# Optimization experiments

Hardware: AMD Instinct MI355X
Metric: run time of the kernel (lower is better)

## Reference

```python
import jax, jax.numpy as jnp
import numpy as np

N, E, D_IN, HID, OUT, H = 20000, 320000, 128, 128, 128, 4

def _lin(key, fan_in, fan_out):
    kw, kb = jax.random.split(key)
    W = jax.random.normal(kw, (fan_in, fan_out), jnp.float32) * 0.05
    b = jax.random.normal(kb, (fan_out,), jnp.float32) * 0.05
    return W, b

def setup_inputs() -> dict:
    key = jax.random.key(0)
    ks = jax.random.split(key, 10)
    x = jax.random.normal(ks[0], (N, D_IN), jnp.float32)
    edge_index = jax.random.randint(ks[1], (2, E), 0, N, jnp.int32)
    # Layer 0: TransformerConv(D_IN -> HID, heads=H, concat=True)
    Wq0, bq0 = _lin(ks[2], D_IN, H * HID)
    Wk0, bk0 = _lin(ks[3], D_IN, H * HID)
    Wv0, bv0 = _lin(ks[4], D_IN, H * HID)
    Ws0, bs0 = _lin(ks[5], D_IN, H * HID)   # root/skip projection
    # Layer 1: TransformerConv(H*HID -> OUT, heads=H, concat=False)
    Wq1, bq1 = _lin(ks[6], H * HID, H * OUT)
    Wk1, bk1 = _lin(ks[7], H * HID, H * OUT)
    Wv1, bv1 = _lin(ks[8], H * HID, H * OUT)
    Ws1, bs1 = _lin(ks[9], H * HID, OUT)    # skip maps to OUT when concat=False
    return dict(x=x, edge_index=edge_index,
                Wq0=Wq0, bq0=bq0, Wk0=Wk0, bk0=bk0, Wv0=Wv0, bv0=bv0, Ws0=Ws0, bs0=bs0,
                Wq1=Wq1, bq1=bq1, Wk1=Wk1, bk1=bk1, Wv1=Wv1, bv1=bv1, Ws1=Ws1, bs1=bs1)

def _transformer_conv(x, src, dst, Wq, bq, Wk, bk, Wv, bv, Ws, bs, heads, out_ch, concat):
    n = x.shape[0]
    q = (x @ Wq + bq).reshape(n, heads, out_ch)
    k = (x @ Wk + bk).reshape(n, heads, out_ch)
    v = (x @ Wv + bv).reshape(n, heads, out_ch)
    # per-edge attention logits: [E, H]
    alpha = jnp.einsum('ehc,ehc->eh', q[dst], k[src]) / jnp.sqrt(jnp.float32(out_ch))
    # softmax grouped by destination node (numerically stable)
    m = jax.ops.segment_max(alpha, dst, num_segments=n)        # [N, H]
    alpha = jnp.exp(alpha - m[dst])
    s = jax.ops.segment_sum(alpha, dst, num_segments=n)       # [N, H]
    alpha = alpha / (s[dst] + 1e-16)
    # weighted scatter-add of messages: [N, H, C]
    out = jax.ops.segment_sum(alpha[..., None] * v[src], dst, num_segments=n)
    if concat:
        out = out.reshape(n, heads * out_ch)
    else:
        out = out.mean(axis=1)
    return out + x @ Ws + bs  # root weight (skip connection)

def reference(x, edge_index,
              Wq0, bq0, Wk0, bk0, Wv0, bv0, Ws0, bs0,
              Wq1, bq1, Wk1, bk1, Wv1, bv1, Ws1, bs1):
    src, dst = edge_index[0], edge_index[1]
    h = _transformer_conv(x, src, dst, Wq0, bq0, Wk0, bk0, Wv0, bv0, Ws0, bs0, H, HID, True)
    h = jax.nn.relu(h)  # dropout is identity in eval mode
    out = _transformer_conv(h, src, dst, Wq1, bq1, Wk1, bk1, Wv1, bv1, Ws1, bs1, H, OUT, False)
    return out
```

## Files before the change

kernel.cpp:

```cpp
#include <hip/hip_runtime.h>
#include <hip/hip_bf16.h>
#include <math.h>

#define HCH    512
#define OUTD   128
#define N0CAT  2048
#define N1CAT  1664
#define P0STR  1024
#define P1STR  640
#define KVW    1024
#define DCAP   64

typedef __attribute__((ext_vector_type(8))) short short8v;
typedef __attribute__((ext_vector_type(8))) unsigned short ushort8v;
typedef __attribute__((ext_vector_type(4))) unsigned short ushort4v;
typedef __attribute__((ext_vector_type(4))) float floatx4;
typedef __attribute__((ext_vector_type(2))) float floatx2;
typedef __attribute__((ext_vector_type(4))) unsigned int uintx4;

__device__ inline float bf2f(unsigned short u) {
    return __uint_as_float(((unsigned)u) << 16);
}

__device__ inline unsigned short f2bf(float f) {
    return (unsigned short)__bfloat16_as_ushort(__float2bfloat16(f));
}

template <bool HI>
__device__ inline floatx2 fp8x2_to_f32(unsigned int w) {
    return __builtin_amdgcn_cvt_pk_f32_fp8(w, HI);
}

__device__ inline unsigned int f32x4_to_fp8(float a, float b, float c, float d) {
    int w = __builtin_amdgcn_cvt_pk_fp8_f32(a, b, 0, false);
    w = __builtin_amdgcn_cvt_pk_fp8_f32(c, d, w, true);
    return (unsigned int)w;
}

__device__ inline void gload_lds16(const void* g, void* l) {
    __builtin_amdgcn_global_load_lds(
        (const __attribute__((address_space(1))) unsigned int*)g,
        (__attribute__((address_space(3))) unsigned int*)l, 16, 0, 0);
}


__global__ void bucket_kernel(const int* __restrict__ src, const int* __restrict__ dst,
                              int* __restrict__ deg, int* __restrict__ srcs, int E) {
    int e = blockIdx.x * 256 + threadIdx.x;
    if (e < E) {
        int d = dst[e];
        int pos = atomicAdd(&deg[d], 1);
        if (pos < DCAP) srcs[d * DCAP + pos] = src[e];
    }
}


__global__ void cast_bf16_kernel(const float* __restrict__ in, __hip_bfloat16* __restrict__ out, int n) {
    int i = blockIdx.x * 256 + threadIdx.x;
    if (i < n) out[i] = __float2bfloat16(in[i]);
}

__global__ __launch_bounds__(256) void tpose4_kernel(const float* __restrict__ W0,
                                                     const float* __restrict__ W1,
                                                     const float* __restrict__ W2,
                                                     const float* __restrict__ W3,
                                                     __hip_bfloat16* __restrict__ out,
                                                     int K, int C) {
    __shared__ float tile[32][33];
    int z = blockIdx.z;
    const float* W = (z == 0) ? W0 : (z == 1) ? W1 : (z == 2) ? W2 : W3;
    __hip_bfloat16* o = out + (size_t)z * C * K;
    int c0 = blockIdx.x * 32, k0 = blockIdx.y * 32;
    int tx = threadIdx.x & 31, ty = threadIdx.x >> 5;
    #pragma unroll
    for (int r = ty; r < 32; r += 8)
        tile[r][tx] = W[(size_t)(k0 + r) * C + c0 + tx];
    __syncthreads();
    #pragma unroll
    for (int r = ty; r < 32; r += 8)
        o[(size_t)(c0 + r) * K + k0 + tx] = __float2bfloat16(tile[tx][r]);
}

__global__ void biascat_kernel(const float* __restrict__ bq0, const float* __restrict__ bk0,
                               const float* __restrict__ bv0, const float* __restrict__ bs0,
                               const float* __restrict__ bq1, const float* __restrict__ bk1,
                               const float* __restrict__ bv1, const float* __restrict__ bs1,
                               float* __restrict__ bc0, float* __restrict__ bc1) {
    int i = blockIdx.x * 256 + threadIdx.x;
    if (i < N0CAT) {
        int sel = i >> 9, col = i & 511;
        const float* b = (sel == 0) ? bq0 : (sel == 1) ? bk0 : (sel == 2) ? bv0 : bs0;
        bc0[i] = b[col];
    }
    if (i < N1CAT) {
        if (i < 1536) {
            int sel = i >> 9, col = i & 511;
            const float* b = (sel == 0) ? bq1 : (sel == 1) ? bk1 : bv1;
            bc1[i] = b[col];
        } else {
            bc1[i] = bs1[i - 1536];
        }
    }
}


#define BM 128
#define BN 128
#define BK 64

__global__ __launch_bounds__(256) void gemm_mfma(const __hip_bfloat16* __restrict__ A,
                                                 const __hip_bfloat16* __restrict__ Bt,
                                                 const float* __restrict__ bias,
                                                 __hip_bfloat16* __restrict__ P,
                                                 int pstride,
                                                 unsigned char* __restrict__ KV8,
                                                 int M, int K, int Nd, int mt_pad) {
    __shared__ __hip_bfloat16 As[BM][BK];
    __shared__ __hip_bfloat16 Bs[BN][BK];
    int f = blockIdx.x;
    int mt = f % mt_pad, nt = f / mt_pad;
    int bm = mt * BM, bn = nt * BN;
    if (bm >= M) return;
    int t = threadIdx.x;
    int lane = t & 63, w = t >> 6;
    int quad = lane >> 4, l16 = lane & 15;
    int wm = (w >> 1) * 64, wn = (w & 1) * 64;

    int srow = w * 8 + (lane >> 3);
    int c8g = (lane & 7) ^ ((lane >> 3) & 7);
    const char* Ab = (const char*)(A + (size_t)(bm + srow) * K + c8g * 8);
    const char* Bb = (const char*)(Bt + (size_t)(bn + srow) * K + c8g * 8);
    char* Al = (char*)&As[0][0] + w * 1024;
    char* Bl = (char*)&Bs[0][0] + w * 1024;

    int sw = l16 & 7;

    floatx4 acc[4][4];
    #pragma unroll
    for (int i = 0; i < 4; i++)
        #pragma unroll
        for (int j = 0; j < 4; j++)
            acc[i][j] = (floatx4)0.0f;

    for (int k0 = 0; k0 < K; k0 += BK) {
        __syncthreads();
        #pragma unroll
        for (int i = 0; i < 4; i++) {
            size_t go = ((size_t)i * 32 * K + k0) * 2;
            gload_lds16(Ab + go, Al + i * 4096);
            gload_lds16(Bb + go, Bl + i * 4096);
        }
        __syncthreads();
        #pragma unroll
        for (int ks = 0; ks < BK; ks += 32) {
            int c8a = (quad + (ks >> 3)) ^ sw;
            short8v af[4], bfr[4];
            #pragma unroll
            for (int i = 0; i < 4; i++)
                af[i] = *(const short8v*)&As[wm + i * 16 + l16][c8a * 8];
            #pragma unroll
            for (int j = 0; j < 4; j++)
                bfr[j] = *(const short8v*)&Bs[wn + j * 16 + l16][c8a * 8];
            #pragma unroll
            for (int i = 0; i < 4; i++)
                #pragma unroll
                for (int j = 0; j < 4; j++)
                    acc[i][j] = __builtin_amdgcn_mfma_f32_16x16x32_bf16(bfr[j], af[i], acc[i][j], 0, 0, 0);
        }
    }

    #pragma unroll
    for (int i = 0; i < 4; i++) {
        int row = bm + wm + i * 16 + l16;
        if (row >= M) continue;
        #pragma unroll
        for (int j = 0; j < 4; j++) {
            int col = bn + wn + j * 16 + quad * 4;
            floatx4 bv = *(const floatx4*)(bias + col);
            float v0 = acc[i][j][0] + bv[0];
            float v1 = acc[i][j][1] + bv[1];
            float v2 = acc[i][j][2] + bv[2];
            float v3 = acc[i][j][3] + bv[3];
            if (col < 512) {
                ushort4v o = { f2bf(v0), f2bf(v1), f2bf(v2), f2bf(v3) };
                *(ushort4v*)(P + (size_t)row * pstride + col) = o;
            } else if (col < 1024) {
                int b = col - 512;
                int nb = ((b >> 3) << 4) + (b & 7);
                *(unsigned int*)(KV8 + (size_t)row * KVW + nb) = f32x4_to_fp8(v0, v1, v2, v3);
            } else if (col < 1536) {
                int b = col - 1024;
                int nb = ((b >> 3) << 4) + 8 + (b & 7);
                *(unsigned int*)(KV8 + (size_t)row * KVW + nb) = f32x4_to_fp8(v0, v1, v2, v3);
            } else {
                ushort4v o = { f2bf(v0), f2bf(v1), f2bf(v2), f2bf(v3) };
                *(ushort4v*)(P + (size_t)row * pstride + 512 + (col - 1536)) = o;
            }
        }
    }
}


#define PF 4

__global__ __launch_bounds__(256) void attn_kernel(const __hip_bfloat16* __restrict__ P,
                                                   int pstride,
                                                   const unsigned char* __restrict__ KV8,
                                                   const int* __restrict__ deg,
                                                   const int* __restrict__ srcs,
                                                   __hip_bfloat16* __restrict__ out_b,
                                                   float* __restrict__ out_f,
                                                   int n_nodes, int mode) {
    int wave = threadIdx.x >> 6;
    int lane = threadIdx.x & 63;
    int node = blockIdx.x * 4 + wave;
    if (node >= n_nodes) return;
    const float scale = 0.08838834764831845f;

    const __hip_bfloat16* Prow = P + (size_t)node * pstride;
    float qf[8];
    {
        ushort8v qu = *(const ushort8v*)(Prow + lane * 8);
        #pragma unroll
        for (int j = 0; j < 8; j++) qf[j] = bf2f(qu[j]) * scale;
    }

    float l = 0.f;
    float acc[8] = {0.f, 0.f, 0.f, 0.f, 0.f, 0.f, 0.f, 0.f};

    int cnt = deg[node];
    if (cnt > DCAP) cnt = DCAP;
    const int* ep = srcs + (size_t)node * DCAP;
    const unsigned char* Kb = KV8 + lane * 16;

    uintx4 kv[PF];
    #pragma unroll
    for (int i = 0; i < PF; i++) {
        if (i < cnt) {
            int s = ep[i];
            kv[i] = *(const uintx4*)(Kb + (size_t)s * KVW);
        }
    }

    int e = 0;
    for (; e + PF <= cnt; e += PF) {
        #pragma unroll
        for (int i = 0; i < PF; i++) {
            uintx4 u = kv[i];
            int pe = e + i + PF;
            if (pe < cnt) {
                int s = ep[pe];
                kv[i] = *(const uintx4*)(Kb + (size_t)s * KVW);
            }
            floatx2 k01 = fp8x2_to_f32<false>(u[0]);
            floatx2 k23 = fp8x2_to_f32<true >(u[0]);
            floatx2 k45 = fp8x2_to_f32<false>(u[1]);
            floatx2 k67 = fp8x2_to_f32<true >(u[1]);
            float part = qf[0] * k01[0] + qf[1] * k01[1]
                       + qf[2] * k23[0] + qf[3] * k23[1]
                       + qf[4] * k45[0] + qf[5] * k45[1]
                       + qf[6] * k67[0] + qf[7] * k67[1];
            part += __shfl_xor(part, 1);
            part += __shfl_xor(part, 2);
            part += __shfl_xor(part, 4);
            part += __shfl_xor(part, 8);
            float p = __expf(part);
            l += p;
            floatx2 v01 = fp8x2_to_f32<false>(u[2]);
            floatx2 v23 = fp8x2_to_f32<true >(u[2]);
            floatx2 v45 = fp8x2_to_f32<false>(u[3]);
            floatx2 v67 = fp8x2_to_f32<true >(u[3]);
            acc[0] += p * v01[0];
            acc[1] += p * v01[1];
            acc[2] += p * v23[0];
            acc[3] += p * v23[1];
            acc[4] += p * v45[0];
            acc[5] += p * v45[1];
            acc[6] += p * v67[0];
            acc[7] += p * v67[1];
        }
    }
    #pragma unroll
    for (int i = 0; i < PF; i++) {
        if (e + i < cnt) {
            uintx4 u = kv[i];
            floatx2 k01 = fp8x2_to_f32<false>(u[0]);
            floatx2 k23 = fp8x2_to_f32<true >(u[0]);
            floatx2 k45 = fp8x2_to_f32<false>(u[1]);
            floatx2 k67 = fp8x2_to_f32<true >(u[1]);
            float part = qf[0] * k01[0] + qf[1] * k01[1]
                       + qf[2] * k23[0] + qf[3] * k23[1]
                       + qf[4] * k45[0] + qf[5] * k45[1]
                       + qf[6] * k67[0] + qf[7] * k67[1];
            part += __shfl_xor(part, 1);
            part += __shfl_xor(part, 2);
            part += __shfl_xor(part, 4);
            part += __shfl_xor(part, 8);
            float p = __expf(part);
            l += p;
            floatx2 v01 = fp8x2_to_f32<false>(u[2]);
            floatx2 v23 = fp8x2_to_f32<true >(u[2]);
            floatx2 v45 = fp8x2_to_f32<false>(u[3]);
            floatx2 v67 = fp8x2_to_f32<true >(u[3]);
            acc[0] += p * v01[0];
            acc[1] += p * v01[1];
            acc[2] += p * v23[0];
            acc[3] += p * v23[1];
            acc[4] += p * v45[0];
            acc[5] += p * v45[1];
            acc[6] += p * v67[0];
            acc[7] += p * v67[1];
        }
    }
    float inv = (l > 0.f) ? 1.f / l : 0.f;

    if (mode == 0) {
        ushort8v su = *(const ushort8v*)(Prow + 512 + lane * 8);
        ushort8v o;
        #pragma unroll
        for (int j = 0; j < 8; j++) {
            float r = fmaxf(acc[j] * inv + bf2f(su[j]), 0.f);
            o[j] = f2bf(r);
        }
        *(ushort8v*)(out_b + (size_t)node * HCH + lane * 8) = o;
    } else {
        float r[8];
        #pragma unroll
        for (int j = 0; j < 8; j++) {
            r[j] = acc[j] * inv;
            r[j] += __shfl_xor(r[j], 16);
            r[j] += __shfl_xor(r[j], 32);
            r[j] *= 0.25f;
        }
        if (lane < 16) {
            const __hip_bfloat16* sp = Prow + 512 + lane * 8;
            float* op = out_f + (size_t)node * OUTD + lane * 8;
            #pragma unroll
            for (int j = 0; j < 8; j++) op[j] = r[j] + bf2f(__bfloat16_as_ushort(sp[j]));
        }
    }
}


static inline size_t align256(size_t x) { return (x + 255) & ~(size_t)255; }

extern "C" void kernel_launch(void* const* d_in, const int* in_sizes, int n_in,
                              void* d_out, int out_size, void* d_ws, size_t ws_size,
                              hipStream_t stream) {
    const float* x   = (const float*)d_in[0];
    const int*   ei  = (const int*)d_in[1];
    const float* Wq0 = (const float*)d_in[2];  const float* bq0 = (const float*)d_in[3];
    const float* Wk0 = (const float*)d_in[4];  const float* bk0 = (const float*)d_in[5];
    const float* Wv0 = (const float*)d_in[6];  const float* bv0 = (const float*)d_in[7];
    const float* Ws0 = (const float*)d_in[8];  const float* bs0 = (const float*)d_in[9];
    const float* Wq1 = (const float*)d_in[10]; const float* bq1 = (const float*)d_in[11];
    const float* Wk1 = (const float*)d_in[12]; const float* bk1 = (const float*)d_in[13];
    const float* Wv1 = (const float*)d_in[14]; const float* bv1 = (const float*)d_in[15];
    const float* Ws1 = (const float*)d_in[16]; const float* bs1 = (const float*)d_in[17];
    float* out = (float*)d_out;

    const int N = in_sizes[0] / 128;
    const int E = in_sizes[1] / 2;
    const int* src = ei;
    const int* dst = ei + E;

    int mtiles = (N + BM - 1) / BM;
    int mt_pad = (mtiles + 7) & ~7;
    const int Mpad = mt_pad * BM;

    char* ws = (char*)d_ws;
    __hip_bfloat16* P0  = (__hip_bfloat16*)ws; ws += align256((size_t)N * P0STR * 2);
    __hip_bfloat16* P1  = P0;
    __hip_bfloat16* Hbb = (__hip_bfloat16*)ws; ws += align256((size_t)Mpad * HCH * 2);
    __hip_bfloat16* Xb  = (__hip_bfloat16*)ws; ws += align256((size_t)Mpad * 128 * 2);
    unsigned char* KV8  = (unsigned char*)ws;  ws += align256((size_t)N * KVW);
    __hip_bfloat16* Wc0 = (__hip_bfloat16*)ws; ws += align256((size_t)N0CAT * 128 * 2);
    __hip_bfloat16* Wc1 = (__hip_bfloat16*)ws; ws += align256((size_t)N1CAT * 512 * 2);
    float* bc0 = (float*)ws; ws += align256((size_t)N0CAT * 4);
    float* bc1 = (float*)ws; ws += align256((size_t)N1CAT * 4);
    int* deg    = (int*)ws; ws += align256((size_t)N * 4);
    int* srcs   = (int*)ws; ws += align256((size_t)N * DCAP * 4);

    dim3 blk(256);

    (void)hipMemsetAsync(deg, 0, (size_t)N * 4, stream);
    bucket_kernel<<<(E + 255) / 256, 256, 0, stream>>>(src, dst, deg, srcs, E);

    cast_bf16_kernel<<<((size_t)N * 128 + 255) / 256, blk, 0, stream>>>(x, Xb, N * 128);
    tpose4_kernel<<<dim3(512 / 32, 128 / 32, 4), blk, 0, stream>>>(Wq0, Wk0, Wv0, Ws0, Wc0, 128, 512);
    tpose4_kernel<<<dim3(512 / 32, 512 / 32, 3), blk, 0, stream>>>(Wq1, Wk1, Wv1, Wv1, Wc1, 512, 512);
    tpose4_kernel<<<dim3(128 / 32, 512 / 32, 1), blk, 0, stream>>>(Ws1, Ws1, Ws1, Ws1, Wc1 + (size_t)1536 * 512, 512, 128);
    biascat_kernel<<<(N0CAT + 255) / 256, blk, 0, stream>>>(bq0, bk0, bv0, bs0, bq1, bk1, bv1, bs1, bc0, bc1);

    gemm_mfma<<<dim3(mt_pad * (N0CAT / BN)), blk, 0, stream>>>(
        Xb, Wc0, bc0, P0, P0STR, KV8, N, 128, N0CAT, mt_pad);
    attn_kernel<<<(N + 3) / 4, blk, 0, stream>>>(P0, P0STR, KV8, deg, srcs, Hbb, nullptr, N, 0);

    gemm_mfma<<<dim3(mt_pad * (N1CAT / BN)), blk, 0, stream>>>(
        Hbb, Wc1, bc1, P1, P1STR, KV8, N, 512, N1CAT, mt_pad);
    attn_kernel<<<(N + 3) / 4, blk, 0, stream>>>(P1, P1STR, KV8, deg, srcs, nullptr, out, N, 1);
}
```

Before: 341.9 us.

## Fuse prep kernels into one launch and process two edges per wave in attention

Merges the x cast, weight transposes, bias concatenation and degree zeroing into a single prep_all kernel, replacing the memset and five launches. This cuts launch and inter-kernel gap overhead. The attention kernel is also restructured so each half-wave handles a different edge with 32 bytes per lane, giving two edges per iteration and a shorter shuffle reduction. The cost is more registers per lane and a reduction across halves at the end.

```diff
diff --git a/kernel.cpp b/kernel.cpp
--- a/kernel.cpp
+++ b/kernel.cpp
@@ -55,23 +55,10 @@
 }
 
 
-__global__ void cast_bf16_kernel(const float* __restrict__ in, __hip_bfloat16* __restrict__ out, int n) {
-    int i = blockIdx.x * 256 + threadIdx.x;
-    if (i < n) out[i] = __float2bfloat16(in[i]);
-}
-
-__global__ __launch_bounds__(256) void tpose4_kernel(const float* __restrict__ W0,
-                                                     const float* __restrict__ W1,
-                                                     const float* __restrict__ W2,
-                                                     const float* __restrict__ W3,
-                                                     __hip_bfloat16* __restrict__ out,
-                                                     int K, int C) {
-    __shared__ float tile[32][33];
-    int z = blockIdx.z;
-    const float* W = (z == 0) ? W0 : (z == 1) ? W1 : (z == 2) ? W2 : W3;
-    __hip_bfloat16* o = out + (size_t)z * C * K;
-    int c0 = blockIdx.x * 32, k0 = blockIdx.y * 32;
-    int tx = threadIdx.x & 31, ty = threadIdx.x >> 5;
+__device__ void tpose_tile(const float* __restrict__ W, __hip_bfloat16* __restrict__ o,
+                           int K, int C, int bx, int by, int t, float (*tile)[33]) {
+    int c0 = bx * 32, k0 = by * 32;
+    int tx = t & 31, ty = t >> 5;
     #pragma unroll
     for (int r = ty; r < 32; r += 8)
         tile[r][tx] = W[(size_t)(k0 + r) * C + c0 + tx];
@@ -81,25 +68,70 @@
         o[(size_t)(c0 + r) * K + k0 + tx] = __float2bfloat16(tile[tx][r]);
 }
 
-__global__ void biascat_kernel(const float* __restrict__ bq0, const float* __restrict__ bk0,
-                               const float* __restrict__ bv0, const float* __restrict__ bs0,
-                               const float* __restrict__ bq1, const float* __restrict__ bk1,
-                               const float* __restrict__ bv1, const float* __restrict__ bs1,
-                               float* __restrict__ bc0, float* __restrict__ bc1) {
-    int i = blockIdx.x * 256 + threadIdx.x;
-    if (i < N0CAT) {
-        int sel = i >> 9, col = i & 511;
-        const float* b = (sel == 0) ? bq0 : (sel == 1) ? bk0 : (sel == 2) ? bv0 : bs0;
-        bc0[i] = b[col];
-    }
-    if (i < N1CAT) {
-        if (i < 1536) {
+__global__ __launch_bounds__(256) void prep_all(
+        const float* __restrict__ x, __hip_bfloat16* __restrict__ Xb,
+        const float* __restrict__ Wq0, const float* __restrict__ Wk0,
+        const float* __restrict__ Wv0, const float* __restrict__ Ws0,
+        const float* __restrict__ Wq1, const float* __restrict__ Wk1,
+        const float* __restrict__ Wv1, const float* __restrict__ Ws1,
+        const float* __restrict__ bq0, const float* __restrict__ bk0,
+        const float* __restrict__ bv0, const float* __restrict__ bs0,
+        const float* __restrict__ bq1, const float* __restrict__ bk1,
+        const float* __restrict__ bv1, const float* __restrict__ bs1,
+        __hip_bfloat16* __restrict__ Wc0, __hip_bfloat16* __restrict__ Wc1,
+        float* __restrict__ bc0, float* __restrict__ bc1,
+        int* __restrict__ deg, int N) {
+    __shared__ float tile[32][33];
+    int t = threadIdx.x;
+    int b = blockIdx.x;
+    int nb_cast = (N * 128 + 255) >> 8;
+    if (b < nb_cast) {
+        int i = b * 256 + t;
+        if (i < N * 128) Xb[i] = __float2bfloat16(x[i]);
+        return;
+    }
+    b -= nb_cast;
+    if (b < 256) {
+        int z = b >> 6, rem = b & 63;
+        const float* W = (z == 0) ? Wq0 : (z == 1) ? Wk0 : (z == 2) ? Wv0 : Ws0;
+        tpose_tile(W, Wc0 + (size_t)z * 512 * 128, 128, 512, rem & 15, rem >> 4, t, tile);
+        return;
+    }
+    b -= 256;
+    if (b < 768) {
+        int z = b >> 8, rem = b & 255;
+        const float* W = (z == 0) ? Wq1 : (z == 1) ? Wk1 : Wv1;
+        tpose_tile(W, Wc1 + (size_t)z * 512 * 512, 512, 512, rem & 15, rem >> 4, t, tile);
+        return;
+    }
+    b -= 768;
+    if (b < 64) {
+        tpose_tile(Ws1, Wc1 + (size_t)1536 * 512, 512, 128, b & 3, b >> 2, t, tile);
+        return;
+    }
+    b -= 64;
+    if (b < 8) {
+        int i = b * 256 + t;
+        if (i < N0CAT) {
             int sel = i >> 9, col = i & 511;
-            const float* b = (sel == 0) ? bq1 : (sel == 1) ? bk1 : bv1;
-            bc1[i] = b[col];
-        } else {
-            bc1[i] = bs1[i - 1536];
-        }
+            const float* bb = (sel == 0) ? bq0 : (sel == 1) ? bk0 : (sel == 2) ? bv0 : bs0;
+            bc0[i] = bb[col];
+        }
+        if (i < N1CAT) {
+            if (i < 1536) {
+                int sel = i >> 9, col = i & 511;
+                const float* bb = (sel == 0) ? bq1 : (sel == 1) ? bk1 : bv1;
+                bc1[i] = bb[col];
+            } else {
+                bc1[i] = bs1[i - 1536];
+            }
+        }
+        return;
+    }
+    b -= 8;
+    {
+        int i = b * 256 + t;
+        if (i < N) deg[i] = 0;
     }
 }
 
@@ -201,7 +233,7 @@
 }
 
 
-#define PF 4
+#define PF2 2
 
 __global__ __launch_bounds__(256) void attn_kernel(const __hip_bfloat16* __restrict__ P,
                                                    int pstride,
@@ -213,130 +245,117 @@
                                                    int n_nodes, int mode) {
     int wave = threadIdx.x >> 6;
     int lane = threadIdx.x & 63;
+    int half = lane >> 5;
+    int li = lane & 31;
     int node = blockIdx.x * 4 + wave;
     if (node >= n_nodes) return;
     const float scale = 0.08838834764831845f;
 
     const __hip_bfloat16* Prow = P + (size_t)node * pstride;
-    float qf[8];
+    float qf[16];
     {
-        ushort8v qu = *(const ushort8v*)(Prow + lane * 8);
-        #pragma unroll
-        for (int j = 0; j < 8; j++) qf[j] = bf2f(qu[j]) * scale;
+        ushort8v q0 = *(const ushort8v*)(Prow + li * 16);
+        ushort8v q1 = *(const ushort8v*)(Prow + li * 16 + 8);
+        #pragma unroll
+        for (int j = 0; j < 8; j++) {
+            qf[j] = bf2f(q0[j]) * scale;
+            qf[8 + j] = bf2f(q1[j]) * scale;
+        }
     }
 
     float l = 0.f;
-    float acc[8] = {0.f, 0.f, 0.f, 0.f, 0.f, 0.f, 0.f, 0.f};
+    float acc[16];
+    #pragma unroll
+    for (int j = 0; j < 16; j++) acc[j] = 0.f;
 
     int cnt = deg[node];
     if (cnt > DCAP) cnt = DCAP;
     const int* ep = srcs + (size_t)node * DCAP;
-    const unsigned char* Kb = KV8 + lane * 16;
-
-    uintx4 kv[PF];
-    #pragma unroll
-    for (int i = 0; i < PF; i++) {
-        if (i < cnt) {
-            int s = ep[i];
-            kv[i] = *(const uintx4*)(Kb + (size_t)s * KVW);
-        }
-    }
-
-    int e = 0;
-    for (; e + PF <= cnt; e += PF) {
-        #pragma unroll
-        for (int i = 0; i < PF; i++) {
-            uintx4 u = kv[i];
-            int pe = e + i + PF;
-            if (pe < cnt) {
-                int s = ep[pe];
-                kv[i] = *(const uintx4*)(Kb + (size_t)s * KVW);
+    const unsigned char* Kb = KV8 + li * 32;
+
+    int npairs = (cnt + 1) >> 1;
+    uintx4 ua[PF2], ub[PF2];
+    #pragma unroll
+    for (int i = 0; i < PF2; i++) {
+        int ei = 2 * i + half;
+        int s = (ei < cnt) ? ep[ei] : 0;
+        const unsigned char* kp = Kb + (size_t)s * KVW;
+        ua[i] = *(const uintx4*)kp;
+        ub[i] = *(const uintx4*)(kp + 16);
+    }
+
+    for (int pi = 0; pi < npairs; pi++) {
+        int slot = pi & (PF2 - 1);
+        uintx4 u0 = ua[slot], u1 = ub[slot];
+        int pe = 2 * (pi + PF2) + half;
+        int sp = (pe < cnt) ? ep[pe] : 0;
+        const unsigned char* kp = Kb + (size_t)sp * KVW;
+        ua[slot] = *(const uintx4*)kp;
+        ub[slot] = *(const uintx4*)(kp + 16);
+
+        floatx2 c;
+        float part;
+        c = fp8x2_to_f32<false>(u0[0]); part  = qf[0] * c[0] + qf[1] * c[1];
+        c = fp8x2_to_f32<true >(u0[0]); part += qf[2] * c[0] + qf[3] * c[1];
+        c = fp8x2_to_f32<false>(u0[1]); part += qf[4] * c[0] + qf[5] * c[1];
+        c = fp8x2_to_f32<true >(u0[1]); part += qf[6] * c[0] + qf[7] * c[1];
+        c = fp8x2_to_f32<false>(u1[0]); part += qf[8] * c[0] + qf[9] * c[1];
+        c = fp8x2_to_f32<true >(u1[0]); part += qf[10] * c[0] + qf[11] * c[1];
+        c = fp8x2_to_f32<false>(u1[1]); part += qf[12] * c[0] + qf[13] * c[1];
+        c = fp8x2_to_f32<true >(u1[1]); part += qf[14] * c[0] + qf[15] * c[1];
+        part += __shfl_xor(part, 1);
+        part += __shfl_xor(part, 2);
+        part += __shfl_xor(part, 4);
+        int ei = 2 * pi + half;
+        float p = (ei < cnt) ? __expf(part) : 0.f;
+        l += p;
+        c = fp8x2_to_f32<false>(u0[2]); acc[0] += p * c[0]; acc[1] += p * c[1];
+        c = fp8x2_to_f32<true >(u0[2]); acc[2] += p * c[0]; acc[3] += p * c[1];
+        c = fp8x2_to_f32<false>(u0[3]); acc[4] += p * c[0]; acc[5] += p * c[1];
+        c = fp8x2_to_f32<true >(u0[3]); acc[6] += p * c[0]; acc[7] += p * c[1];
+        c = fp8x2_to_f32<false>(u1[2]); acc[8] += p * c[0]; acc[9] += p * c[1];
+        c = fp8x2_to_f32<true >(u1[2]); acc[10] += p * c[0]; acc[11] += p * c[1];
+        c = fp8x2_to_f32<false>(u1[3]); acc[12] += p * c[0]; acc[13] += p * c[1];
+        c = fp8x2_to_f32<true >(u1[3]); acc[14] += p * c[0]; acc[15] += p * c[1];
+    }
+
+    l += __shfl_xor(l, 32);
+    #pragma unroll
+    for (int j = 0; j < 16; j++) acc[j] += __shfl_xor(acc[j], 32);
+    float inv = (l > 0.f) ? 1.f / l : 0.f;
+
+    if (mode == 0) {
+        const __hip_bfloat16* sp = Prow + 512 + li * 16 + half * 8;
+        ushort8v su = *(const ushort8v*)sp;
+        ushort8v o;
+        #pragma unroll
+        for (int j = 0; j < 8; j++) {
+            float r = fmaxf(acc[8 * half + j] * inv + bf2f(su[j]), 0.f);
+            o[j] = f2bf(r);
+        }
+        *(ushort8v*)(out_b + (size_t)node * HCH + li * 16 + half * 8) = o;
+    } else {
+        float r[16];
+        #pragma unroll
+        for (int j = 0; j < 16; j++) {
+            r[j] = acc[j] * inv;
+            r[j] += __shfl_xor(r[j], 8);
+            r[j] += __shfl_xor(r[j], 16);
+            r[j] *= 0.25f;
+        }
+        if (li < 8) {
+            int c0 = 16 * li + 8 * half;
+            const __hip_bfloat16* sp = Prow + 512 + c0;
+            ushort8v su = *(const ushort8v*)sp;
+            float* op = out_f + (size_t)node * OUTD + c0;
+            floatx4 o0, o1;
+            #pragma unroll
+            for (int j = 0; j < 4; j++) {
+                o0[j] = r[8 * half + j] + bf2f(su[j]);
+                o1[j] = r[8 * half + 4 + j] + bf2f(su[4 + j]);
             }
-            floatx2 k01 = fp8x2_to_f32<false>(u[0]);
-            floatx2 k23 = fp8x2_to_f32<true >(u[0]);
-            floatx2 k45 = fp8x2_to_f32<false>(u[1]);
-            floatx2 k67 = fp8x2_to_f32<true >(u[1]);
-            float part = qf[0] * k01[0] + qf[1] * k01[1]
-                       + qf[2] * k23[0] + qf[3] * k23[1]
-                       + qf[4] * k45[0] + qf[5] * k45[1]
-                       + qf[6] * k67[0] + qf[7] * k67[1];
-            part += __shfl_xor(part, 1);
-            part += __shfl_xor(part, 2);
-            part += __shfl_xor(part, 4);
-            part += __shfl_xor(part, 8);
-            float p = __expf(part);
-            l += p;
-            floatx2 v01 = fp8x2_to_f32<false>(u[2]);
-            floatx2 v23 = fp8x2_to_f32<true >(u[2]);
-            floatx2 v45 = fp8x2_to_f32<false>(u[3]);
-            floatx2 v67 = fp8x2_to_f32<true >(u[3]);
-            acc[0] += p * v01[0];
-            acc[1] += p * v01[1];
-            acc[2] += p * v23[0];
-            acc[3] += p * v23[1];
-            acc[4] += p * v45[0];
-            acc[5] += p * v45[1];
-            acc[6] += p * v67[0];
-            acc[7] += p * v67[1];
-        }
-    }
-    #pragma unroll
-    for (int i = 0; i < PF; i++) {
-        if (e + i < cnt) {
-            uintx4 u = kv[i];
-            floatx2 k01 = fp8x2_to_f32<false>(u[0]);
-            floatx2 k23 = fp8x2_to_f32<true >(u[0]);
-            floatx2 k45 = fp8x2_to_f32<false>(u[1]);
-            floatx2 k67 = fp8x2_to_f32<true >(u[1]);
-            float part = qf[0] * k01[0] + qf[1] * k01[1]
-                       + qf[2] * k23[0] + qf[3] * k23[1]
-                       + qf[4] * k45[0] + qf[5] * k45[1]
-                       + qf[6] * k67[0] + qf[7] * k67[1];
-            part += __shfl_xor(part, 1);
-            part += __shfl_xor(part, 2);
-            part += __shfl_xor(part, 4);
-            part += __shfl_xor(part, 8);
-            float p = __expf(part);
-            l += p;
-            floatx2 v01 = fp8x2_to_f32<false>(u[2]);
-            floatx2 v23 = fp8x2_to_f32<true >(u[2]);
-            floatx2 v45 = fp8x2_to_f32<false>(u[3]);
-            floatx2 v67 = fp8x2_to_f32<true >(u[3]);
-            acc[0] += p * v01[0];
-            acc[1] += p * v01[1];
-            acc[2] += p * v23[0];
-            acc[3] += p * v23[1];
-            acc[4] += p * v45[0];
-            acc[5] += p * v45[1];
-            acc[6] += p * v67[0];
-            acc[7] += p * v67[1];
-        }
-    }
-    float inv = (l > 0.f) ? 1.f / l : 0.f;
-
-    if (mode == 0) {
-        ushort8v su = *(const ushort8v*)(Prow + 512 + lane * 8);
-        ushort8v o;
-        #pragma unroll
-        for (int j = 0; j < 8; j++) {
-            float r = fmaxf(acc[j] * inv + bf2f(su[j]), 0.f);
-            o[j] = f2bf(r);
-        }
-        *(ushort8v*)(out_b + (size_t)node * HCH + lane * 8) = o;
-    } else {
-        float r[8];
-        #pragma unroll
-        for (int j = 0; j < 8; j++) {
-            r[j] = acc[j] * inv;
-            r[j] += __shfl_xor(r[j], 16);
-            r[j] += __shfl_xor(r[j], 32);
-            r[j] *= 0.25f;
-        }
-        if (lane < 16) {
-            const __hip_bfloat16* sp = Prow + 512 + lane * 8;
-            float* op = out_f + (size_t)node * OUTD + lane * 8;
-            #pragma unroll
-            for (int j = 0; j < 8; j++) op[j] = r[j] + bf2f(__bfloat16_as_ushort(sp[j]));
+            *(floatx4*)op = o0;
+            *(floatx4*)(op + 4) = o1;
         }
     }
 }
@@ -383,14 +402,15 @@
 
     dim3 blk(256);
 
-    (void)hipMemsetAsync(deg, 0, (size_t)N * 4, stream);
+    int nb_cast = (N * 128 + 255) / 256;
+    int nb_deg = (N + 255) / 256;
+    int nb_prep = nb_cast + 256 + 768 + 64 + 8 + nb_deg;
+    prep_all<<<nb_prep, blk, 0, stream>>>(
+        x, Xb, Wq0, Wk0, Wv0, Ws0, Wq1, Wk1, Wv1, Ws1,
+        bq0, bk0, bv0, bs0, bq1, bk1, bv1, bs1,
+        Wc0, Wc1, bc0, bc1, deg, N);
+
     bucket_kernel<<<(E + 255) / 256, 256, 0, stream>>>(src, dst, deg, srcs, E);
-
-    cast_bf16_kernel<<<((size_t)N * 128 + 255) / 256, blk, 0, stream>>>(x, Xb, N * 128);
-    tpose4_kernel<<<dim3(512 / 32, 128 / 32, 4), blk, 0, stream>>>(Wq0, Wk0, Wv0, Ws0, Wc0, 128, 512);
-    tpose4_kernel<<<dim3(512 / 32, 512 / 32, 3), blk, 0, stream>>>(Wq1, Wk1, Wv1, Wv1, Wc1, 512, 512);
-    tpose4_kernel<<<dim3(128 / 32, 512 / 32, 1), blk, 0, stream>>>(Ws1, Ws1, Ws1, Ws1, Wc1 + (size_t)1536 * 512, 512, 128);
-    biascat_kernel<<<(N0CAT + 255) / 256, blk, 0, stream>>>(bq0, bk0, bv0, bs0, bq1, bk1, bv1, bs1, bc0, bc1);
 
     gemm_mfma<<<dim3(mt_pad * (N0CAT / BN)), blk, 0, stream>>>(
         Xb, Wc0, bc0, P0, P0STR, KV8, N, 128, N0CAT, mt_pad);
```

After: 373.4 us. +9.2%, slower.
